# Optimization experiments

Hardware: AMD Instinct MI355X
Metric: run time of the kernel (lower is better)

Reference implementation:

```python
import jax, jax.numpy as jnp
import numpy as np

B, N, C = 64, 197, 768
H = 12
D = C // H
SCALE = D ** -0.5
TAU = 5.0
THRESHOLD = 0.6
NEG_INF = float('-inf')


def setup_inputs() -> dict:
    key = jax.random.key(0)
    ks = jax.random.split(key, 10)
    def gumbel(k, shape):
        # -log(Exponential) == standard Gumbel noise, matches torch exponential_().log()
        e = jax.random.exponential(k, shape, dtype=jnp.float32)
        return -jnp.log(e + 1e-10)
    s = 0.02
    return {
        'x': jax.random.normal(ks[0], (B, N, C), dtype=jnp.float32),
        'g1': gumbel(ks[1], (B, N - 1, 1)),
        'g2': gumbel(ks[2], (B, N - 1, 1)),
        'Wq': jax.random.normal(ks[3], (C, C), dtype=jnp.float32) * s,
        'Wk': jax.random.normal(ks[4], (C, C), dtype=jnp.float32) * s,
        'Wv': jax.random.normal(ks[5], (C, C), dtype=jnp.float32) * s,
        'Wp': jax.random.normal(ks[6], (C, C), dtype=jnp.float32) * s,
        'bp': jnp.zeros((C,), dtype=jnp.float32),
        'Wm': jax.random.normal(ks[7], (1, C), dtype=jnp.float32) * s,
        'bm': jnp.zeros((1,), dtype=jnp.float32),
    }


def reference(x, g1, g2, Wq, Wk, Wv, Wp, bp, Wm, bm):
    b, n, c = x.shape
    # QKV projections (qkv_bias=False), reshape to (B, H, N, D)
    q = (x @ Wq.T).reshape(b, n, H, D).transpose(0, 2, 1, 3)
    k = (x @ Wk.T).reshape(b, n, H, D).transpose(0, 2, 1, 3)
    v = (x @ Wv.T).reshape(b, n, H, D).transpose(0, 2, 1, 3)

    attn_pre = jnp.einsum('bhnd,bhmd->bhnm', q, k) * SCALE  # (B,H,N,N)

    # SimpleTokenSelect: gumbel-sigmoid gating on non-CLS tokens (training=True, hard=True)
    logits = x[:, 1:] @ Wm.T + bm                       # (B, N-1, 1)
    y_soft = jax.nn.sigmoid((logits + g1 - g2) / TAU)
    y_hard = (y_soft > THRESHOLD).astype(y_soft.dtype)
    ts = y_hard - jax.lax.stop_gradient(y_soft) + y_soft  # straight-through
    ts = jnp.concatenate([jnp.ones((b, 1, 1), dtype=ts.dtype), ts], axis=1)[..., 0]  # (B, N)

    # attention policy = outer product of token gates, detached (ada_token_detach_attn)
    policy = jax.lax.stop_gradient(jnp.einsum('bn,bm->bnm', ts, ts))[:, None]  # (B,1,N,N)

    # pre-softmax masking: zero gated scores, -inf off-diagonal entries of gated rows
    eye = jnp.eye(n, dtype=attn_pre.dtype)
    neg_mask = jnp.where(1.0 - policy - eye > 0, NEG_INF, 0.0)
    attn = jax.nn.softmax(attn_pre * policy + neg_mask, axis=-1)

    out = jnp.einsum('bhnm,bhmd->bhnd', attn, v)        # (B,H,N,D)
    out = out.transpose(0, 2, 1, 3).reshape(b, n, c)
    out = out @ Wp.T + bp                                # proj (dropout p=0)
    return out
```

## Files before the change

kernel.cpp:

```cpp
#include <hip/hip_runtime.h>
#include <hip/hip_bf16.h>
#include <cstdint>

typedef unsigned short u16;
typedef __attribute__((ext_vector_type(8))) short bf16x8;
typedef __attribute__((ext_vector_type(4))) float f32x4;

#define NB 64
#define NN 197
#define NC 768
#define NH 12
#define ND 64
#define NM (NB*NN)
#define CAP 96
#define NT 24
#define SELR 6144
#define MSELT 48
#define ASZ ((size_t)NM*NC)
#define WSZ ((size_t)NC*NC)
#define SELSZ2 ((size_t)SELR*NC)

#define WAITVM(N) asm volatile("s_waitcnt vmcnt(" #N ")" ::: "memory")
#define SBAR() __builtin_amdgcn_s_barrier()
#define SCHEDB() __builtin_amdgcn_sched_barrier(0)

__device__ __forceinline__ u16 f2bf(float f) {
  uint32_t u = __float_as_uint(f);
  u += 0x7fffu + ((u >> 16) & 1u);
  return (u16)(u >> 16);
}

__device__ __forceinline__ void gl_lds16(const u16* g, u16* l) {
  __builtin_amdgcn_global_load_lds(
      (const __attribute__((address_space(1))) void*)g,
      (__attribute__((address_space(3))) void*)l, 16, 0, 0);
}

#define GATEB 3152
#define WBLK 576
#define TRBLK 144
__global__ __launch_bounds__(256) void k1_prep(const float* __restrict__ x,
    const float* __restrict__ g1, const float* __restrict__ g2,
    const float* __restrict__ Wm, const float* __restrict__ bm,
    const float* __restrict__ wq, const float* __restrict__ wk,
    const float* __restrict__ wv, const float* __restrict__ wp,
    u16* __restrict__ xb, u16* __restrict__ wqb, u16* __restrict__ wkb,
    u16* __restrict__ wvb, u16* __restrict__ wpb, u16* __restrict__ wvt,
    float* __restrict__ ts) {
  __shared__ u16 T[64][72];
  int bid = blockIdx.x, tid = threadIdx.x;

  if (bid < GATEB) {
    int wave = tid >> 6, lane = tid & 63;
    int wid = bid * 4 + wave;
    int b = wid / NN, n = wid % NN;
    const float* xr = x + (size_t)wid * NC;
    u16* xbr = xb + (size_t)wid * NC;
    double acc = 0.0;
    #pragma unroll
    for (int i = 0; i < 3; ++i) {
      float4 f = *(const float4*)(xr + lane * 4 + 256 * i);
      float4 w = *(const float4*)(Wm + lane * 4 + 256 * i);
      acc += (double)f.x * w.x + (double)f.y * w.y
           + (double)f.z * w.z + (double)f.w * w.w;
      ushort4 o;
      o.x = f2bf(f.x); o.y = f2bf(f.y); o.z = f2bf(f.z); o.w = f2bf(f.w);
      *(ushort4*)(xbr + lane * 4 + 256 * i) = o;
    }
    #pragma unroll
    for (int off = 32; off; off >>= 1) acc += __shfl_down(acc, off);
    float o = 1.0f;
    if (n != 0) {
      double z = (acc + (double)bm[0] + (double)g1[b*(NN-1) + n - 1]
                                      - (double)g2[b*(NN-1) + n - 1]) / 5.0;
      o = (z > 0.4054651081081643820) ? 1.0f : 0.0f;
    }
    if (lane == 0) ts[wid] = o;
    return;
  }
  bid -= GATEB;
  if (bid < 4*WBLK) {
    int seg = bid / WBLK;
    int i = (bid - seg * WBLK) * 256 + tid;
    const float* src; u16* dst;
    if (seg == 0)      { src = wq; dst = wqb; }
    else if (seg == 1) { src = wk; dst = wkb; }
    else if (seg == 2) { src = wv; dst = wvb; }
    else               { src = wp; dst = wpb; }
    float4 f = ((const float4*)src)[i];
    ushort4 o;
    o.x = f2bf(f.x); o.y = f2bf(f.y); o.z = f2bf(f.z); o.w = f2bf(f.w);
    ((ushort4*)dst)[i] = o;
    return;
  }
  bid -= 4*WBLK;
  {
    int bx = bid % 12, by = bid / 12;
    int j0 = by * 64, k0 = bx * 64;
    #pragma unroll
    for (int g = 0; g < 4; ++g) {
      int r = g * 16 + (tid >> 4);
      int c4 = (tid & 15) * 4;
      float4 f = *(const float4*)(wv + (size_t)(j0 + r) * NC + k0 + c4);
      T[c4 + 0][r] = f2bf(f.x);
      T[c4 + 1][r] = f2bf(f.y);
      T[c4 + 2][r] = f2bf(f.z);
      T[c4 + 3][r] = f2bf(f.w);
    }
    __syncthreads();
    #pragma unroll
    for (int g = 0; g < 4; ++g) {
      int r = g * 16 + (tid >> 4);
      int c4 = (tid & 15) * 4;
      ushort4 o = *(ushort4*)&T[r][c4];
      *(ushort4*)(wvt + (size_t)(k0 + r) * NC + j0 + c4) = o;
    }
  }
}

__global__ __launch_bounds__(256) void ck_compact(const float* __restrict__ ts,
    int* __restrict__ cnt, int* __restrict__ boff, int* __restrict__ gidx) {
  __shared__ unsigned long long bm[4];
  __shared__ int runoff;
  int tid = threadIdx.x, lane = tid & 63, wave = tid >> 6;
  if (tid == 0) runoff = 0;
  __syncthreads();
  for (int b = 0; b < NB; ++b) {
    bool sel = (tid < NN) && (ts[b * NN + tid] > 0.5f);
    unsigned long long m = __ballot(sel);
    if (lane == 0) bm[wave] = m;
    __syncthreads();
    int before = 0, total = 0;
    #pragma unroll
    for (int w = 0; w < 4; ++w) {
      int c = __popcll(bm[w]);
      total += c;
      if (w < wave) before += c;
    }
    int within = __popcll(bm[wave] & ((lane == 0) ? 0ull : (~0ull >> (64 - lane))));
    int pos = before + within;
    int cc = total < CAP ? total : CAP;
    int base = runoff;
    if (sel && pos < CAP) gidx[base + pos] = b * NN + tid;
    __syncthreads();
    if (tid == 0) { cnt[b] = cc; boff[b] = base; runoff = base + cc; }
    __syncthreads();
  }
  int tot = runoff;
  if (tid == 0) boff[NB] = tot;
  for (int i = tot + tid; i < SELR; i += 256) gidx[i] = 0;
}

__global__ __launch_bounds__(256) void k2_wvp_qkv(const u16* __restrict__ xb,
    const u16* __restrict__ wq3, const u16* __restrict__ wpb,
    const u16* __restrict__ wvt, u16* __restrict__ wvpb,
    u16* __restrict__ sel3, const int* __restrict__ boff,
    const int* __restrict__ gidx) {
  alignas(16) __shared__ u16 SA[3][128][32];
  alignas(16) __shared__ u16 SB[3][128][32];
  int bid = blockIdx.x;
  int tid = threadIdx.x, lane = tid & 63, wave = tid >> 6;
  int lr = lane & 15, lg = lane >> 4, lk = lg * 8;

  if (bid < MSELT * 18) {
    int mt = bid / 18, r18 = bid % 18;
    int z = r18 / 6, y = r18 % 6;
    int total = boff[NB];
    int m0 = mt * 128;
    if (m0 >= total) return;
    const u16* W = wq3 + (size_t)z * WSZ;
    u16* o = sel3 + (size_t)z * SELSZ2;
    int n0 = y * 128;
    int wr = (wave >> 1) * 64, wc = (wave & 1) * 64;

    int id0 = (wave*2 + 0) * 64 + lane, id1 = (wave*2 + 1) * 64 + lane;
    const u16* baseA0 = xb + (size_t)gidx[m0 + (id0 >> 2)] * NC + (id0 & 3) * 8;
    const u16* baseA1 = xb + (size_t)gidx[m0 + (id1 >> 2)] * NC + (id1 & 3) * 8;
    const u16* baseB0 = W + (size_t)(n0 + (id0 >> 2)) * NC + (id0 & 3) * 8;
    const u16* baseB1 = W + (size_t)(n0 + (id1 >> 2)) * NC + (id1 & 3) * 8;
    u16* dA0 = &SA[0][0][0] + (size_t)(wave*2 + 0) * 512;
    u16* dA1 = &SA[0][0][0] + (size_t)(wave*2 + 1) * 512;
    u16* dB0 = &SB[0][0][0] + (size_t)(wave*2 + 0) * 512;
    u16* dB1 = &SB[0][0][0] + (size_t)(wave*2 + 1) * 512;

    f32x4 acc[4][4];
    #pragma unroll
    for (int i = 0; i < 4; ++i)
      #pragma unroll
      for (int j = 0; j < 4; ++j) acc[i][j] = (f32x4){0.f,0.f,0.f,0.f};

    for (int k0 = 0; k0 < NC; k0 += 32) {
      gl_lds16(baseA0 + k0, dA0);
      gl_lds16(baseA1 + k0, dA1);
      gl_lds16(baseB0 + k0, dB0);
      gl_lds16(baseB1 + k0, dB1);
      __syncthreads();
      bf16x8 af[4], bfr[4];
      #pragma unroll
      for (int f = 0; f < 4; ++f) {
        af[f]  = *(const bf16x8*)(&SA[0][wr + f*16 + lr][lk]);
        bfr[f] = *(const bf16x8*)(&SB[0][wc + f*16 + lr][lk]);
      }
      #pragma unroll
      for (int i = 0; i < 4; ++i)
        #pragma unroll
        for (int j = 0; j < 4; ++j)
          acc[i][j] = __builtin_amdgcn_mfma_f32_16x16x32_bf16(af[i], bfr[j], acc[i][j], 0, 0, 0);
      __syncthreads();
    }
    #pragma unroll
    for (int i = 0; i < 4; ++i) {
      int rbase = m0 + wr + i*16 + 4*lg;
      #pragma unroll
      for (int j = 0; j < 4; ++j) {
        int col = n0 + wc + j*16 + lr;
        #pragma unroll
        for (int r = 0; r < 4; ++r) {
          int row = rbase + r;
          if (row < total)
            o[(size_t)row * NC + col] = f2bf(acc[i][j][r]);
        }
      }
    }
    return;
  }

  int wb = bid - MSELT * 18;
  int m0 = (wb / 6) * 128, n0 = (wb % 6) * 128;
  int wr = (wave >> 1) * 64, wc = (wave & 1) * 64;
  f32x4 acc[4][4];
  #pragma unroll
  for (int i = 0; i < 4; ++i)
    #pragma unroll
    for (int j = 0; j < 4; ++j) acc[i][j] = (f32x4){0.f,0.f,0.f,0.f};
  auto stage = [&](int buf, int kt) {
    int k0 = kt * 32;
    #pragma unroll
    for (int i = 0; i < 2; ++i) {
      int c = wave * 2 + i;
      int id = c * 64 + lane;
      int row = id >> 2, col8 = (id & 3) * 8;
      gl_lds16(wpb + (size_t)(m0 + row) * NC + k0 + col8, &SA[buf][0][0] + c * 512);
      gl_lds16(wvt + (size_t)(n0 + row) * NC + k0 + col8, &SB[buf][0][0] + c * 512);
    }
  };
  auto comp = [&](int buf) {
    bf16x8 af[4], bfr[4];
    #pragma unroll
    for (int f = 0; f < 4; ++f) {
      af[f]  = *(const bf16x8*)(&SA[buf][wr + f*16 + lr][lk]);
      bfr[f] = *(const bf16x8*)(&SB[buf][wc + f*16 + lr][lk]);
    }
    #pragma unroll
    for (int i = 0; i < 4; ++i)
      #pragma unroll
      for (int j = 0; j < 4; ++j)
        acc[i][j] = __builtin_amdgcn_mfma_f32_16x16x32_bf16(af[i], bfr[j], acc[i][j], 0, 0, 0);
  };
  stage(0, 0); stage(1, 1);
  int cb = 0;
  for (int t = 0; t < NT; ++t) {
    if (t + 2 < NT) {
      int sb = cb + 2; if (sb > 2) sb -= 3;
      stage(sb, t + 2);
      WAITVM(8);
    } else if (t + 1 < NT) { WAITVM(4); }
    else { WAITVM(0); }
    SBAR(); SCHEDB();
    comp(cb);
    SBAR();
    cb = (cb == 2) ? 0 : cb + 1;
  }
  #pragma unroll
  for (int i = 0; i < 4; ++i)
    #pragma unroll
    for (int j = 0; j < 4; ++j)
      #pragma unroll
      for (int r = 0; r < 4; ++r)
        wvpb[(size_t)(m0 + wr + i*16 + 4*lg + r) * NC + n0 + wc + j*16 + lr] =
            f2bf(acc[i][j][r]);
}

__global__ __launch_bounds__(256) void attn_sel(const u16* __restrict__ qsel,
    const u16* __restrict__ ksel, const u16* __restrict__ vsel,
    u16* __restrict__ zsel, const int* __restrict__ cnt,
    const int* __restrict__ boff) {
  alignas(16) __shared__ u16 Vt[64][232];
  int bh = blockIdx.x;
  int b = bh / NH, h = bh % NH;
  int cntb = cnt[b];
  int boffb = boff[b];
  int tid = threadIdx.x, lane = tid & 63, wave = tid >> 6;
  int lr = lane & 15, lg = lane >> 4;
  const size_t qbase = (size_t)boffb * NC + (size_t)h * ND;

  for (int id = tid; id < cntb * 8; id += 256) {
    int i = id >> 3, c8 = (id & 7) * 8;
    int4 val = *(const int4*)(vsel + qbase + (size_t)i * NC + c8);
    u16 tmp[8];
    *(int4*)tmp = val;
    #pragma unroll
    for (int e = 0; e < 8; ++e) Vt[c8 + e][i] = tmp[e];
  }
  for (int id = tid; id < 64 * 32; id += 256)
    Vt[id >> 5][cntb + (id & 31)] = 0;
  __syncthreads();

  int nchunk = (cntb + 15) >> 4;
  int mtmax  = nchunk;
  int mcmax  = (cntb + 31) >> 5;
  int idx0 = (((lane & 15) | ((lane & 16) << 1))) << 2;
  int idx1 = idx0 + 64;

  for (int qc = wave; qc < nchunk; qc += 4) {
    const u16* qp = qsel + qbase + (size_t)(qc * 16 + lr) * NC + lg * 8;
    bf16x8 qf0 = *(const bf16x8*)(qp);
    bf16x8 qf1 = *(const bf16x8*)(qp + 32);

    f32x4 s[6];
    #pragma unroll
    for (int mt = 0; mt < 6; ++mt) s[mt] = (f32x4){0.f,0.f,0.f,0.f};
    #pragma unroll
    for (int mt = 0; mt < 6; ++mt) {
      if (mt < mtmax) {
        const u16* kp = ksel + qbase + (size_t)(mt * 16 + lr) * NC + lg * 8;
        bf16x8 kf0 = *(const bf16x8*)(kp);
        bf16x8 kf1 = *(const bf16x8*)(kp + 32);
        f32x4 a = (f32x4){0.f,0.f,0.f,0.f};
        a = __builtin_amdgcn_mfma_f32_16x16x32_bf16(kf0, qf0, a, 0, 0, 0);
        a = __builtin_amdgcn_mfma_f32_16x16x32_bf16(kf1, qf1, a, 0, 0, 0);
        s[mt] = a;
      }
    }

    float mx = -3e38f;
    #pragma unroll
    for (int mt = 0; mt < 6; ++mt)
      #pragma unroll
      for (int jj = 0; jj < 4; ++jj) {
        int mm = mt*16 + 4*lg + jj;
        float val = (mm < cntb) ? s[mt][jj] * 0.125f : -1e30f;
        s[mt][jj] = val;
        mx = fmaxf(mx, val);
      }
    mx = fmaxf(mx, __shfl_xor(mx, 16));
    mx = fmaxf(mx, __shfl_xor(mx, 32));
    float sum = 0.f;
    #pragma unroll
    for (int mt = 0; mt < 6; ++mt)
      #pragma unroll
      for (int jj = 0; jj < 4; ++jj) {
        float pv = __expf(s[mt][jj] - mx);
        s[mt][jj] = pv;
        sum += pv;
      }
    sum += __shfl_xor(sum, 16);
    sum += __shfl_xor(sum, 32);
    float inv = 1.0f / sum;

    uint32_t u[6][2];
    #pragma unroll
    for (int mt = 0; mt < 6; ++mt) {
      u[mt][0] = ((uint32_t)f2bf(s[mt][1]*inv) << 16) | f2bf(s[mt][0]*inv);
      u[mt][1] = ((uint32_t)f2bf(s[mt][3]*inv) << 16) | f2bf(s[mt][2]*inv);
    }

    f32x4 oacc[4];
    #pragma unroll
    for (int dt = 0; dt < 4; ++dt) oacc[dt] = (f32x4){0.f,0.f,0.f,0.f};
    #pragma unroll
    for (int mc = 0; mc < 3; ++mc) {
      if (mc < mcmax) {
        uint32_t a0 = (uint32_t)__builtin_amdgcn_ds_bpermute(idx0, (int)u[2*mc][0]);
        uint32_t b0 = (uint32_t)__builtin_amdgcn_ds_bpermute(idx0, (int)u[2*mc+1][0]);
        uint32_t a1 = (uint32_t)__builtin_amdgcn_ds_bpermute(idx0, (int)u[2*mc][1]);
        uint32_t b1 = (uint32_t)__builtin_amdgcn_ds_bpermute(idx0, (int)u[2*mc+1][1]);
        uint32_t a2 = (uint32_t)__builtin_amdgcn_ds_bpermute(idx1, (int)u[2*mc][0]);
        uint32_t b2 = (uint32_t)__builtin_amdgcn_ds_bpermute(idx1, (int)u[2*mc+1][0]);
        uint32_t a3 = (uint32_t)__builtin_amdgcn_ds_bpermute(idx1, (int)u[2*mc][1]);
        uint32_t b3 = (uint32_t)__builtin_amdgcn_ds_bpermute(idx1, (int)u[2*mc+1][1]);
        bool hi = (lg >= 2);
        union { uint32_t w[4]; bf16x8 v; } pu;
        pu.w[0] = hi ? b0 : a0;
        pu.w[1] = hi ? b1 : a1;
        pu.w[2] = hi ? b2 : a2;
        pu.w[3] = hi ? b3 : a3;
        bf16x8 pa = pu.v;
        #pragma unroll
        for (int dt = 0; dt < 4; ++dt) {
          bf16x8 vf = *(const bf16x8*)(&Vt[dt*16 + lr][mc*32 + lg*8]);
          oacc[dt] = __builtin_amdgcn_mfma_f32_16x16x32_bf16(pa, vf, oacc[dt], 0, 0, 0);
        }
      }
    }

    #pragma unroll
    for (int r = 0; r < 4; ++r) {
      int nloc = qc*16 + 4*lg + r;
      if (nloc < cntb) {
        u16* op = zsel + qbase + (size_t)nloc * NC + lr;
        #pragma unroll
        for (int dt = 0; dt < 4; ++dt)
          op[dt*16] = f2bf(oacc[dt][r]);
      }
    }
  }
}

#define DBLK 594
#define PJBLK (MSELT*6)
__global__ __launch_bounds__(256) void k4_out(const u16* __restrict__ xb,
    const u16* __restrict__ wvpb, const u16* __restrict__ zsel,
    const u16* __restrict__ wpb, const float* __restrict__ ts,
    const float* __restrict__ bp, float* __restrict__ out,
    const int* __restrict__ boff, const int* __restrict__ gidx) {
  alignas(16) __shared__ u16 SA[128][32];
  alignas(16) __shared__ u16 SB[128][32];
  int bid = blockIdx.x;
  int tid = threadIdx.x, lane = tid & 63, wave = tid >> 6;
  int lr = lane & 15, lg = lane >> 4, lk = lg * 8;
  int wr = (wave >> 1) * 64, wc = (wave & 1) * 64;

  const u16* Abase; const u16* Bbase;
  int m0, n0, total = 0;
  bool dense = (bid < DBLK);
  if (dense) {
    int xcd = bid & 7, loc = bid >> 3;
    int wgid = (xcd < 2 ? xcd * 75 : 150 + (xcd - 2) * 74) + loc;
    m0 = (wgid / 6) * 128;
    n0 = (wgid % 6) * 128;
    Abase = xb; Bbase = wvpb;
  } else {
    int pid = bid - DBLK;
    int mt = pid / 6, y = pid % 6;
    total = boff[NB];
    m0 = mt * 128;
    if (m0 >= total) return;
    n0 = y * 128;
    Abase = zsel; Bbase = wpb;
  }

  int id0 = (wave*2 + 0) * 64 + lane, id1 = (wave*2 + 1) * 64 + lane;
  const u16* baseA0 = Abase + (size_t)(m0 + (id0 >> 2)) * NC + (id0 & 3) * 8;
  const u16* baseA1 = Abase + (size_t)(m0 + (id1 >> 2)) * NC + (id1 & 3) * 8;
  const u16* baseB0 = Bbase + (size_t)(n0 + (id0 >> 2)) * NC + (id0 & 3) * 8;
  const u16* baseB1 = Bbase + (size_t)(n0 + (id1 >> 2)) * NC + (id1 & 3) * 8;
  u16* dA0 = &SA[0][0] + (size_t)(wave*2 + 0) * 512;
  u16* dA1 = &SA[0][0] + (size_t)(wave*2 + 1) * 512;
  u16* dB0 = &SB[0][0] + (size_t)(wave*2 + 0) * 512;
  u16* dB1 = &SB[0][0] + (size_t)(wave*2 + 1) * 512;

  f32x4 acc[4][4];
  #pragma unroll
  for (int i = 0; i < 4; ++i)
    #pragma unroll
    for (int j = 0; j < 4; ++j) acc[i][j] = (f32x4){0.f,0.f,0.f,0.f};

  for (int k0 = 0; k0 < NC; k0 += 32) {
    gl_lds16(baseA0 + k0, dA0);
    gl_lds16(baseA1 + k0, dA1);
    gl_lds16(baseB0 + k0, dB0);
    gl_lds16(baseB1 + k0, dB1);
    __syncthreads();
    bf16x8 af[4], bfr[4];
    #pragma unroll
    for (int f = 0; f < 4; ++f) {
      af[f]  = *(const bf16x8*)(&SA[wr + f*16 + lr][lk]);
      bfr[f] = *(const bf16x8*)(&SB[wc + f*16 + lr][lk]);
    }
    #pragma unroll
    for (int i = 0; i < 4; ++i)
      #pragma unroll
      for (int j = 0; j < 4; ++j)
        acc[i][j] = __builtin_amdgcn_mfma_f32_16x16x32_bf16(af[i], bfr[j], acc[i][j], 0, 0, 0);
    __syncthreads();
  }

  if (dense) {
    #pragma unroll
    for (int i = 0; i < 4; ++i) {
      int rbase = m0 + wr + i*16 + 4*lg;
      #pragma unroll
      for (int j = 0; j < 4; ++j) {
        int col = n0 + wc + j*16 + lr;
        #pragma unroll
        for (int r = 0; r < 4; ++r) {
          int row = rbase + r;
          if (row < NM && ts[row] < 0.5f)
            out[(size_t)row * NC + col] = acc[i][j][r] + bp[col];
        }
      }
    }
  } else {
    #pragma unroll
    for (int i = 0; i < 4; ++i) {
      int rbase = m0 + wr + i*16 + 4*lg;
      #pragma unroll
      for (int j = 0; j < 4; ++j) {
        int col = n0 + wc + j*16 + lr;
        #pragma unroll
        for (int r = 0; r < 4; ++r) {
          int row = rbase + r;
          if (row < total) {
            int grow = gidx[row];
            out[(size_t)grow * NC + col] = acc[i][j][r] + bp[col];
          }
        }
      }
    }
  }
}

extern "C" void kernel_launch(void* const* d_in, const int* in_sizes, int n_in,
                              void* d_out, int out_size, void* d_ws, size_t ws_size,
                              hipStream_t stream) {
  const float* x  = (const float*)d_in[0];
  const float* g1 = (const float*)d_in[1];
  const float* g2 = (const float*)d_in[2];
  const float* Wq = (const float*)d_in[3];
  const float* Wk = (const float*)d_in[4];
  const float* Wv = (const float*)d_in[5];
  const float* Wp = (const float*)d_in[6];
  const float* bp = (const float*)d_in[7];
  const float* Wm = (const float*)d_in[8];
  const float* bm = (const float*)d_in[9];
  float* out = (float*)d_out;

  const size_t act_sz = ASZ * 2;
  const size_t w_sz   = WSZ * 2;
  const size_t sel_sz = SELSZ2 * 2;
  size_t need = act_sz + 4*sel_sz + 6*w_sz + (size_t)NM*4
              + (size_t)(NB+1)*4 + (size_t)NB*4 + (size_t)SELR*4 + 256;
  if (ws_size < need) return;

  char* p = (char*)d_ws;
  u16* xb   = (u16*)p; p += act_sz;
  u16* qsel = (u16*)p; p += sel_sz;
  u16* ksel = (u16*)p; p += sel_sz;
  u16* vsel = (u16*)p; p += sel_sz;
  u16* zsel = (u16*)p; p += sel_sz;
  u16* wqb  = (u16*)p; p += w_sz;
  u16* wkb  = (u16*)p; p += w_sz;
  u16* wvb  = (u16*)p; p += w_sz;
  u16* wpb  = (u16*)p; p += w_sz;
  u16* wvtb = (u16*)p; p += w_sz;
  u16* wvpb = (u16*)p; p += w_sz;
  float* ts = (float*)p; p += (size_t)NM*4;
  int* cnt  = (int*)p;  p += (size_t)NB*4;
  int* boff = (int*)p;  p += (size_t)(NB+1)*4;
  int* gidx = (int*)p;
  (void)wkb; (void)wvb;

  k1_prep<<<dim3(GATEB + 4*WBLK + TRBLK), 256, 0, stream>>>(
      x, g1, g2, Wm, bm, Wq, Wk, Wv, Wp,
      xb, wqb, wkb, wvb, wpb, wvtb, ts);

  ck_compact<<<dim3(1), 256, 0, stream>>>(ts, cnt, boff, gidx);

  k2_wvp_qkv<<<dim3(MSELT*18 + 36), 256, 0, stream>>>(
      xb, wqb, wpb, wvtb, wvpb, qsel, boff, gidx);

  attn_sel<<<dim3(NB*NH), 256, 0, stream>>>(qsel, ksel, vsel, zsel, cnt, boff);

  k4_out<<<dim3(DBLK + PJBLK), 256, 0, stream>>>(
      xb, wvpb, zsel, wpb, ts, bp, out, boff, gidx);
}
```

Before: 118.1 us.

## Parallelize token compaction and co-schedule dense output GEMM with attention

The compaction kernel now runs on 1024 threads and handles all batches in parallel with a wave-level prefix scan, replacing the serial per-batch loop. 378 of the dense output GEMM tiles (x @ WvP for unselected tokens) move into a new combined kernel that runs alongside the selected-token attention blocks, so the attention stage no longer leaves the GPU underoccupied. The rest of the dense tiles stay with the projection kernel. The WvP GEMM in k2 loses its triple-buffered pipeline and now shares the simpler single-buffer loop with the selected QKV path, which may slow that part.

```diff
diff --git a/kernel.cpp b/kernel.cpp
--- a/kernel.cpp
+++ b/kernel.cpp
@@ -19,10 +19,6 @@
 #define ASZ ((size_t)NM*NC)
 #define WSZ ((size_t)NC*NC)
 #define SELSZ2 ((size_t)SELR*NC)
-
-#define WAITVM(N) asm volatile("s_waitcnt vmcnt(" #N ")" ::: "memory")
-#define SBAR() __builtin_amdgcn_s_barrier()
-#define SCHEDB() __builtin_amdgcn_sched_barrier(0)
 
 __device__ __forceinline__ u16 f2bf(float f) {
   uint32_t u = __float_as_uint(f);
@@ -118,37 +114,62 @@
   }
 }
 
-__global__ __launch_bounds__(256) void ck_compact(const float* __restrict__ ts,
+__global__ __launch_bounds__(1024) void ck_compact(const float* __restrict__ ts,
     int* __restrict__ cnt, int* __restrict__ boff, int* __restrict__ gidx) {
-  __shared__ unsigned long long bm[4];
-  __shared__ int runoff;
+  __shared__ unsigned long long masks[NB][4];
+  __shared__ int scnt[NB];
+  __shared__ int soff[NB + 1];
   int tid = threadIdx.x, lane = tid & 63, wave = tid >> 6;
-  if (tid == 0) runoff = 0;
+
+  #pragma unroll
+  for (int p = 0; p < 4; ++p) {
+    int b = wave * 4 + p;
+    int count = 0;
+    #pragma unroll
+    for (int c = 0; c < 4; ++c) {
+      int t = c * 64 + lane;
+      bool sel = (t < NN) && (ts[b * NN + t] > 0.5f);
+      unsigned long long m = __ballot(sel);
+      if (lane == 0) masks[b][c] = m;
+      count += __popcll(m);
+    }
+    if (lane == 0) scnt[b] = count < CAP ? count : CAP;
+  }
   __syncthreads();
-  for (int b = 0; b < NB; ++b) {
-    bool sel = (tid < NN) && (ts[b * NN + tid] > 0.5f);
-    unsigned long long m = __ballot(sel);
-    if (lane == 0) bm[wave] = m;
-    __syncthreads();
-    int before = 0, total = 0;
-    #pragma unroll
-    for (int w = 0; w < 4; ++w) {
-      int c = __popcll(bm[w]);
-      total += c;
-      if (w < wave) before += c;
-    }
-    int within = __popcll(bm[wave] & ((lane == 0) ? 0ull : (~0ull >> (64 - lane))));
-    int pos = before + within;
-    int cc = total < CAP ? total : CAP;
-    int base = runoff;
-    if (sel && pos < CAP) gidx[base + pos] = b * NN + tid;
-    __syncthreads();
-    if (tid == 0) { cnt[b] = cc; boff[b] = base; runoff = base + cc; }
-    __syncthreads();
-  }
-  int tot = runoff;
-  if (tid == 0) boff[NB] = tot;
-  for (int i = tot + tid; i < SELR; i += 256) gidx[i] = 0;
+
+  if (wave == 0) {
+    int acc = 0;
+    for (int i = 0; i < NB; ++i) {
+      int v = scnt[i];
+      if (i < lane) acc += v;
+    }
+    soff[lane] = acc;
+    if (lane == 63) soff[NB] = acc + scnt[63];
+  }
+  __syncthreads();
+
+  #pragma unroll
+  for (int p = 0; p < 4; ++p) {
+    int b = wave * 4 + p;
+    int base = soff[b];
+    int cc = scnt[b];
+    int prior = 0;
+    #pragma unroll
+    for (int c = 0; c < 4; ++c) {
+      unsigned long long m = masks[b][c];
+      int t = c * 64 + lane;
+      bool sel = ((m >> lane) & 1ull) != 0;
+      int within = __popcll(m & ((lane == 0) ? 0ull : (~0ull >> (64 - lane))));
+      int pos = prior + within;
+      if (sel && pos < cc) gidx[base + pos] = b * NN + t;
+      prior += __popcll(m);
+    }
+  }
+  if (tid < NB) { cnt[tid] = scnt[tid]; boff[tid] = soff[tid]; }
+  if (tid == NB) boff[NB] = soff[NB];
+  __syncthreads();
+  int total = soff[NB];
+  for (int i = total + tid; i < SELR; i += 1024) gidx[i] = 0;
 }
 
 __global__ __launch_bounds__(256) void k2_wvp_qkv(const u16* __restrict__ xb,
@@ -156,32 +177,129 @@
     const u16* __restrict__ wvt, u16* __restrict__ wvpb,
     u16* __restrict__ sel3, const int* __restrict__ boff,
     const int* __restrict__ gidx) {
-  alignas(16) __shared__ u16 SA[3][128][32];
-  alignas(16) __shared__ u16 SB[3][128][32];
+  alignas(16) __shared__ u16 SA[128][32];
+  alignas(16) __shared__ u16 SB[128][32];
   int bid = blockIdx.x;
   int tid = threadIdx.x, lane = tid & 63, wave = tid >> 6;
   int lr = lane & 15, lg = lane >> 4, lk = lg * 8;
-
-  if (bid < MSELT * 18) {
+  int wr = (wave >> 1) * 64, wc = (wave & 1) * 64;
+
+  int id0 = (wave*2 + 0) * 64 + lane, id1 = (wave*2 + 1) * 64 + lane;
+  const u16 *baseA0, *baseA1, *baseB0, *baseB1;
+  bool isSel = (bid < MSELT * 18);
+  int m0, n0, total = 0, z = 0;
+  if (isSel) {
     int mt = bid / 18, r18 = bid % 18;
-    int z = r18 / 6, y = r18 % 6;
-    int total = boff[NB];
-    int m0 = mt * 128;
+    z = r18 / 6; int y = r18 % 6;
+    total = boff[NB];
+    m0 = mt * 128;
     if (m0 >= total) return;
+    n0 = y * 128;
     const u16* W = wq3 + (size_t)z * WSZ;
+    baseA0 = xb + (size_t)gidx[m0 + (id0 >> 2)] * NC + (id0 & 3) * 8;
+    baseA1 = xb + (size_t)gidx[m0 + (id1 >> 2)] * NC + (id1 & 3) * 8;
+    baseB0 = W + (size_t)(n0 + (id0 >> 2)) * NC + (id0 & 3) * 8;
+    baseB1 = W + (size_t)(n0 + (id1 >> 2)) * NC + (id1 & 3) * 8;
+  } else {
+    int wb = bid - MSELT * 18;
+    m0 = (wb / 6) * 128; n0 = (wb % 6) * 128;
+    baseA0 = wpb + (size_t)(m0 + (id0 >> 2)) * NC + (id0 & 3) * 8;
+    baseA1 = wpb + (size_t)(m0 + (id1 >> 2)) * NC + (id1 & 3) * 8;
+    baseB0 = wvt + (size_t)(n0 + (id0 >> 2)) * NC + (id0 & 3) * 8;
+    baseB1 = wvt + (size_t)(n0 + (id1 >> 2)) * NC + (id1 & 3) * 8;
+  }
+  u16* dA0 = &SA[0][0] + (size_t)(wave*2 + 0) * 512;
+  u16* dA1 = &SA[0][0] + (size_t)(wave*2 + 1) * 512;
+  u16* dB0 = &SB[0][0] + (size_t)(wave*2 + 0) * 512;
+  u16* dB1 = &SB[0][0] + (size_t)(wave*2 + 1) * 512;
+
+  f32x4 acc[4][4];
+  #pragma unroll
+  for (int i = 0; i < 4; ++i)
+    #pragma unroll
+    for (int j = 0; j < 4; ++j) acc[i][j] = (f32x4){0.f,0.f,0.f,0.f};
+
+  for (int k0 = 0; k0 < NC; k0 += 32) {
+    gl_lds16(baseA0 + k0, dA0);
+    gl_lds16(baseA1 + k0, dA1);
+    gl_lds16(baseB0 + k0, dB0);
+    gl_lds16(baseB1 + k0, dB1);
+    __syncthreads();
+    bf16x8 af[4], bfr[4];
+    #pragma unroll
+    for (int f = 0; f < 4; ++f) {
+      af[f]  = *(const bf16x8*)(&SA[wr + f*16 + lr][lk]);
+      bfr[f] = *(const bf16x8*)(&SB[wc + f*16 + lr][lk]);
+    }
+    #pragma unroll
+    for (int i = 0; i < 4; ++i)
+      #pragma unroll
+      for (int j = 0; j < 4; ++j)
+        acc[i][j] = __builtin_amdgcn_mfma_f32_16x16x32_bf16(af[i], bfr[j], acc[i][j], 0, 0, 0);
+    __syncthreads();
+  }
+
+  if (isSel) {
     u16* o = sel3 + (size_t)z * SELSZ2;
-    int n0 = y * 128;
+    #pragma unroll
+    for (int i = 0; i < 4; ++i) {
+      int rbase = m0 + wr + i*16 + 4*lg;
+      #pragma unroll
+      for (int j = 0; j < 4; ++j) {
+        int col = n0 + wc + j*16 + lr;
+        #pragma unroll
+        for (int r = 0; r < 4; ++r) {
+          int row = rbase + r;
+          if (row < total)
+            o[(size_t)row * NC + col] = f2bf(acc[i][j][r]);
+        }
+      }
+    }
+  } else {
+    #pragma unroll
+    for (int i = 0; i < 4; ++i)
+      #pragma unroll
+      for (int j = 0; j < 4; ++j)
+        #pragma unroll
+        for (int r = 0; r < 4; ++r)
+          wvpb[(size_t)(m0 + wr + i*16 + 4*lg + r) * NC + n0 + wc + j*16 + lr] =
+              f2bf(acc[i][j][r]);
+  }
+}
+
+#define DTOT 594
+#define DN1 378
+#define DN2 (DTOT-DN1)
+__global__ __launch_bounds__(256) void k3_dense_attn(const u16* __restrict__ xb,
+    const u16* __restrict__ wvpb, const u16* __restrict__ qsel,
+    const u16* __restrict__ ksel, const u16* __restrict__ vsel,
+    u16* __restrict__ zsel, const float* __restrict__ ts,
+    const float* __restrict__ bp, float* __restrict__ out,
+    const int* __restrict__ cnt, const int* __restrict__ boff) {
+  alignas(16) __shared__ u16 LDSU[64*232];
+  int bid = blockIdx.x;
+  int tid = threadIdx.x, lane = tid & 63, wave = tid >> 6;
+  int lr = lane & 15, lg = lane >> 4;
+
+  if (bid < DN1) {
+    u16 (*SA)[32] = reinterpret_cast<u16(*)[32]>(&LDSU[0]);
+    u16 (*SB)[32] = reinterpret_cast<u16(*)[32]>(&LDSU[4096]);
+    int lk = lg * 8;
     int wr = (wave >> 1) * 64, wc = (wave & 1) * 64;
+    int d = bid;
+    int xcd = d & 7, loc = d >> 3;
+    int wgid = (xcd < 2 ? xcd * 75 : 150 + (xcd - 2) * 74) + loc;
+    int m0 = (wgid / 6) * 128, n0 = (wgid % 6) * 128;
 
     int id0 = (wave*2 + 0) * 64 + lane, id1 = (wave*2 + 1) * 64 + lane;
-    const u16* baseA0 = xb + (size_t)gidx[m0 + (id0 >> 2)] * NC + (id0 & 3) * 8;
-    const u16* baseA1 = xb + (size_t)gidx[m0 + (id1 >> 2)] * NC + (id1 & 3) * 8;
-    const u16* baseB0 = W + (size_t)(n0 + (id0 >> 2)) * NC + (id0 & 3) * 8;
-    const u16* baseB1 = W + (size_t)(n0 + (id1 >> 2)) * NC + (id1 & 3) * 8;
-    u16* dA0 = &SA[0][0][0] + (size_t)(wave*2 + 0) * 512;
-    u16* dA1 = &SA[0][0][0] + (size_t)(wave*2 + 1) * 512;
-    u16* dB0 = &SB[0][0][0] + (size_t)(wave*2 + 0) * 512;
-    u16* dB1 = &SB[0][0][0] + (size_t)(wave*2 + 1) * 512;
+    const u16* baseA0 = xb + (size_t)(m0 + (id0 >> 2)) * NC + (id0 & 3) * 8;
+    const u16* baseA1 = xb + (size_t)(m0 + (id1 >> 2)) * NC + (id1 & 3) * 8;
+    const u16* baseB0 = wvpb + (size_t)(n0 + (id0 >> 2)) * NC + (id0 & 3) * 8;
+    const u16* baseB1 = wvpb + (size_t)(n0 + (id1 >> 2)) * NC + (id1 & 3) * 8;
+    u16* dA0 = &SA[0][0] + (size_t)(wave*2 + 0) * 512;
+    u16* dA1 = &SA[0][0] + (size_t)(wave*2 + 1) * 512;
+    u16* dB0 = &SB[0][0] + (size_t)(wave*2 + 0) * 512;
+    u16* dB1 = &SB[0][0] + (size_t)(wave*2 + 1) * 512;
 
     f32x4 acc[4][4];
     #pragma unroll
@@ -198,8 +316,8 @@
       bf16x8 af[4], bfr[4];
       #pragma unroll
       for (int f = 0; f < 4; ++f) {
-        af[f]  = *(const bf16x8*)(&SA[0][wr + f*16 + lr][lk]);
-        bfr[f] = *(const bf16x8*)(&SB[0][wc + f*16 + lr][lk]);
+        af[f]  = *(const bf16x8*)(&SA[wr + f*16 + lr][lk]);
+        bfr[f] = *(const bf16x8*)(&SB[wc + f*16 + lr][lk]);
       }
       #pragma unroll
       for (int i = 0; i < 4; ++i)
@@ -217,81 +335,19 @@
         #pragma unroll
         for (int r = 0; r < 4; ++r) {
           int row = rbase + r;
-          if (row < total)
-            o[(size_t)row * NC + col] = f2bf(acc[i][j][r]);
+          if (row < NM && ts[row] < 0.5f)
+            out[(size_t)row * NC + col] = acc[i][j][r] + bp[col];
         }
       }
     }
     return;
   }
 
-  int wb = bid - MSELT * 18;
-  int m0 = (wb / 6) * 128, n0 = (wb % 6) * 128;
-  int wr = (wave >> 1) * 64, wc = (wave & 1) * 64;
-  f32x4 acc[4][4];
-  #pragma unroll
-  for (int i = 0; i < 4; ++i)
-    #pragma unroll
-    for (int j = 0; j < 4; ++j) acc[i][j] = (f32x4){0.f,0.f,0.f,0.f};
-  auto stage = [&](int buf, int kt) {
-    int k0 = kt * 32;
-    #pragma unroll
-    for (int i = 0; i < 2; ++i) {
-      int c = wave * 2 + i;
-      int id = c * 64 + lane;
-      int row = id >> 2, col8 = (id & 3) * 8;
-      gl_lds16(wpb + (size_t)(m0 + row) * NC + k0 + col8, &SA[buf][0][0] + c * 512);
-      gl_lds16(wvt + (size_t)(n0 + row) * NC + k0 + col8, &SB[buf][0][0] + c * 512);
-    }
-  };
-  auto comp = [&](int buf) {
-    bf16x8 af[4], bfr[4];
-    #pragma unroll
-    for (int f = 0; f < 4; ++f) {
-      af[f]  = *(const bf16x8*)(&SA[buf][wr + f*16 + lr][lk]);
-      bfr[f] = *(const bf16x8*)(&SB[buf][wc + f*16 + lr][lk]);
-    }
-    #pragma unroll
-    for (int i = 0; i < 4; ++i)
-      #pragma unroll
-      for (int j = 0; j < 4; ++j)
-        acc[i][j] = __builtin_amdgcn_mfma_f32_16x16x32_bf16(af[i], bfr[j], acc[i][j], 0, 0, 0);
-  };
-  stage(0, 0); stage(1, 1);
-  int cb = 0;
-  for (int t = 0; t < NT; ++t) {
-    if (t + 2 < NT) {
-      int sb = cb + 2; if (sb > 2) sb -= 3;
-      stage(sb, t + 2);
-      WAITVM(8);
-    } else if (t + 1 < NT) { WAITVM(4); }
-    else { WAITVM(0); }
-    SBAR(); SCHEDB();
-    comp(cb);
-    SBAR();
-    cb = (cb == 2) ? 0 : cb + 1;
-  }
-  #pragma unroll
-  for (int i = 0; i < 4; ++i)
-    #pragma unroll
-    for (int j = 0; j < 4; ++j)
-      #pragma unroll
-      for (int r = 0; r < 4; ++r)
-        wvpb[(size_t)(m0 + wr + i*16 + 4*lg + r) * NC + n0 + wc + j*16 + lr] =
-            f2bf(acc[i][j][r]);
-}
-
-__global__ __launch_bounds__(256) void attn_sel(const u16* __restrict__ qsel,
-    const u16* __restrict__ ksel, const u16* __restrict__ vsel,
-    u16* __restrict__ zsel, const int* __restrict__ cnt,
-    const int* __restrict__ boff) {
-  alignas(16) __shared__ u16 Vt[64][232];
-  int bh = blockIdx.x;
+  u16 (*Vt)[232] = reinterpret_cast<u16(*)[232]>(&LDSU[0]);
+  int bh = bid - DN1;
   int b = bh / NH, h = bh % NH;
   int cntb = cnt[b];
   int boffb = boff[b];
-  int tid = threadIdx.x, lane = tid & 63, wave = tid >> 6;
-  int lr = lane & 15, lg = lane >> 4;
   const size_t qbase = (size_t)boffb * NC + (size_t)h * ND;
 
   for (int id = tid; id < cntb * 8; id += 256) {
@@ -407,7 +463,6 @@
   }
 }
 
-#define DBLK 594
 #define PJBLK (MSELT*6)
 __global__ __launch_bounds__(256) void k4_out(const u16* __restrict__ xb,
     const u16* __restrict__ wvpb, const u16* __restrict__ zsel,
@@ -423,16 +478,16 @@
 
   const u16* Abase; const u16* Bbase;
   int m0, n0, total = 0;
-  bool dense = (bid < DBLK);
+  bool dense = (bid >= PJBLK);
   if (dense) {
-    int xcd = bid & 7, loc = bid >> 3;
+    int d = DN1 + (bid - PJBLK);
+    int xcd = d & 7, loc = d >> 3;
     int wgid = (xcd < 2 ? xcd * 75 : 150 + (xcd - 2) * 74) + loc;
     m0 = (wgid / 6) * 128;
     n0 = (wgid % 6) * 128;
     Abase = xb; Bbase = wvpb;
   } else {
-    int pid = bid - DBLK;
-    int mt = pid / 6, y = pid % 6;
+    int mt = bid / 6, y = bid % 6;
     total = boff[NB];
     m0 = mt * 128;
     if (m0 >= total) return;
@@ -555,13 +610,14 @@
       x, g1, g2, Wm, bm, Wq, Wk, Wv, Wp,
       xb, wqb, wkb, wvb, wpb, wvtb, ts);
 
-  ck_compact<<<dim3(1), 256, 0, stream>>>(ts, cnt, boff, gidx);
+  ck_compact<<<dim3(1), 1024, 0, stream>>>(ts, cnt, boff, gidx);
 
   k2_wvp_qkv<<<dim3(MSELT*18 + 36), 256, 0, stream>>>(
       xb, wqb, wpb, wvtb, wvpb, qsel, boff, gidx);
 
-  attn_sel<<<dim3(NB*NH), 256, 0, stream>>>(qsel, ksel, vsel, zsel, cnt, boff);
-
-  k4_out<<<dim3(DBLK + PJBLK), 256, 0, stream>>>(
+  k3_dense_attn<<<dim3(DN1 + NB*NH), 256, 0, stream>>>(
+      xb, wvpb, qsel, ksel, vsel, zsel, ts, bp, out, cnt, boff);
+
+  k4_out<<<dim3(PJBLK + DN2), 256, 0, stream>>>(
       xb, wvpb, zsel, wpb, ts, bp, out, boff, gidx);
 }
```

Measured after the change: 113.0 us. 4.4% less time.
